# Performance work log

Hardware: AMD Instinct MI355X
Metric: run time of the kernel (lower is better)

The kernel has to match this reference:

```python
import jax, jax.numpy as jnp
import numpy as np

K = 3          # kernel_size
DEG_P = 6      # numerator coeffs (order 5)
DEG_Q = 4      # denominator coeffs (powers 1..4)


def setup_inputs() -> dict:
    key = jax.random.key(0)
    k1, k2, k3 = jax.random.split(key, 3)
    B, Cin, Cout, H, W = 4, 16, 16, 64, 64
    x = jax.random.normal(k1, (B, Cin, H, W), dtype=jnp.float32)
    # per (out_channel f, in_channel c, kernel position p) rational coefficients
    A = jax.random.normal(k2, (Cout, Cin, K * K, DEG_P), dtype=jnp.float32) * 0.1
    Bc = jax.random.normal(k3, (Cout, Cin, K * K, DEG_Q), dtype=jnp.float32) * 0.1
    return {"x": x, "A": A, "Bc": Bc}


def reference(x, A, Bc):
    # x: [B, C, H, W]; A: [F, C, K*K, 6]; Bc: [F, C, K*K, 4]
    B, C, H, W = x.shape
    pad = (K - 1) // 2
    xp = jnp.pad(x, ((0, 0), (0, 0), (pad, pad), (pad, pad)))
    # sliding windows, one slice per kernel offset -> [K*K, B, C, H, W]
    wins = jnp.stack([xp[:, :, i:i + H, j:j + W]
                      for i in range(K) for j in range(K)])
    # powers x^0..x^5 -> [K*K, B, C, H, W, 6]
    pw = wins[..., None] ** jnp.arange(DEG_P, dtype=x.dtype)
    P = jnp.einsum('pbchwi,fcpi->fpbchw', pw, A)
    Q = 1.0 + jnp.abs(jnp.einsum('pbchwi,fcpi->fpbchw', pw[..., 1:1 + DEG_Q], Bc))
    # sum over kernel positions (p) and input channels (c) -> [F, B, H, W]
    out = jnp.sum(P / Q, axis=(1, 3))
    return jnp.transpose(out, (1, 0, 2, 3))  # [B, F, H, W]
```

## Files before the change

kernel.cpp:

```cpp
#include <hip/hip_runtime.h>


#define BB   4
#define CIN  16
#define COUT 16
#define HH   64
#define WW   64

__global__ __launch_bounds__(256) void KAConv_kernel(
    const float* __restrict__ x,
    const float* __restrict__ A,
    const float* __restrict__ Bc,
    float* __restrict__ out)
{
    const int blk   = blockIdx.x;
    const int htile = blk & 15;
    const int f     = (blk >> 4) & 15;
    const int b     = blk >> 8;

    const int t = threadIdx.x;
    const int w = t & 63;
    const int h = (htile << 2) + (t >> 6);

    const float* __restrict__ xb = x  + b * (CIN * HH * WW);
    const float* __restrict__ Af = A  + f * (CIN * 9 * 6);
    const float* __restrict__ Bf = Bc + f * (CIN * 9 * 4);

    float acc = 0.0f;

    for (int c = 0; c < CIN; ++c) {
        const float* __restrict__ xc = xb + c * (HH * WW);

        float v[9];
        #pragma unroll
        for (int i = 0; i < 3; ++i) {
            const int hh = h + i - 1;
            #pragma unroll
            for (int j = 0; j < 3; ++j) {
                const int ww2 = w + j - 1;
                const bool ok = (hh >= 0) & (hh < HH) & (ww2 >= 0) & (ww2 < WW);
                v[i * 3 + j] = ok ? xc[hh * WW + ww2] : 0.0f;
            }
        }

        const float* __restrict__ Ac = Af + c * (9 * 6);
        const float* __restrict__ Bq = Bf + c * (9 * 4);

        #pragma unroll
        for (int p = 0; p < 9; ++p) {
            const float vv = v[p];
            const float* __restrict__ a  = Ac + p * 6;
            const float* __restrict__ bq = Bq + p * 4;

            float P = a[5];
            P = fmaf(P, vv, a[4]);
            P = fmaf(P, vv, a[3]);
            P = fmaf(P, vv, a[2]);
            P = fmaf(P, vv, a[1]);
            P = fmaf(P, vv, a[0]);

            float Qs = bq[3];
            Qs = fmaf(Qs, vv, bq[2]);
            Qs = fmaf(Qs, vv, bq[1]);
            Qs = fmaf(Qs, vv, bq[0]);
            Qs *= vv;

            const float Q = 1.0f + fabsf(Qs);
            acc = fmaf(P, __builtin_amdgcn_rcpf(Q), acc);
        }
    }

    out[((b * COUT + f) * HH + h) * WW + w] = acc;
}

extern "C" void kernel_launch(void* const* d_in, const int* in_sizes, int n_in,
                              void* d_out, int out_size, void* d_ws, size_t ws_size,
                              hipStream_t stream) {
    const float* x  = (const float*)d_in[0];
    const float* A  = (const float*)d_in[1];
    const float* Bc = (const float*)d_in[2];
    float* out = (float*)d_out;

    const int grid = BB * COUT * (HH / 4);
    KAConv_kernel<<<grid, 256, 0, stream>>>(x, A, Bc, out);
}
```

Measured before the change: 23.77 us.

## Compute two output rows per thread and reorder block index mapping

Each thread now computes two vertically adjacent output rows, loading a 4x3 window instead of two 3x3 windows and reusing the coefficient loads across both rows. The grid is halved (512 blocks), and f becomes the fastest-varying block index so neighbouring blocks share the same x tile. This cuts redundant input and coefficient loads per output and adds ILP, at the cost of fewer blocks (lower occupancy across the 256 CUs) and more registers.

```diff
diff --git a/kernel.cpp b/kernel.cpp
--- a/kernel.cpp
+++ b/kernel.cpp
@@ -14,63 +14,73 @@
     float* __restrict__ out)
 {
     const int blk   = blockIdx.x;
-    const int htile = blk & 15;
-    const int f     = (blk >> 4) & 15;
-    const int b     = blk >> 8;
+    const int f     = blk & 15;
+    const int rtile = (blk >> 4) & 7;
+    const int b     = blk >> 7;
 
-    const int t = threadIdx.x;
-    const int w = t & 63;
-    const int h = (htile << 2) + (t >> 6);
+    const int t    = threadIdx.x;
+    const int w    = t & 63;
+    const int warp = t >> 6;
+    const int r0   = (rtile << 3) + (warp << 1);
+    const int r1   = r0 + 1;
 
     const float* __restrict__ xb = x  + b * (CIN * HH * WW);
     const float* __restrict__ Af = A  + f * (CIN * 9 * 6);
     const float* __restrict__ Bf = Bc + f * (CIN * 9 * 4);
 
-    float acc = 0.0f;
+    float acc0 = 0.0f, acc1 = 0.0f;
 
     for (int c = 0; c < CIN; ++c) {
         const float* __restrict__ xc = xb + c * (HH * WW);
 
-        float v[9];
+        float vv[4][3];
         #pragma unroll
-        for (int i = 0; i < 3; ++i) {
-            const int hh = h + i - 1;
+        for (int ri = 0; ri < 4; ++ri) {
+            const int hh  = r0 - 1 + ri;
+            const bool okh = (hh >= 0) & (hh < HH);
             #pragma unroll
             for (int j = 0; j < 3; ++j) {
-                const int ww2 = w + j - 1;
-                const bool ok = (hh >= 0) & (hh < HH) & (ww2 >= 0) & (ww2 < WW);
-                v[i * 3 + j] = ok ? xc[hh * WW + ww2] : 0.0f;
+                const int wj = w + j - 1;
+                const bool ok = okh & (wj >= 0) & (wj < WW);
+                vv[ri][j] = ok ? xc[hh * WW + wj] : 0.0f;
             }
         }
 
-        const float* __restrict__ Ac = Af + c * (9 * 6);
-        const float* __restrict__ Bq = Bf + c * (9 * 4);
+        const float* __restrict__ Ac = Af + c * 54;
+        const float* __restrict__ Bq = Bf + c * 36;
 
         #pragma unroll
         for (int p = 0; p < 9; ++p) {
-            const float vv = v[p];
+            const int i = p / 3;
+            const int j = p % 3;
+            const float va = vv[i][j];
+            const float vb = vv[i + 1][j];
             const float* __restrict__ a  = Ac + p * 6;
             const float* __restrict__ bq = Bq + p * 4;
 
-            float P = a[5];
-            P = fmaf(P, vv, a[4]);
-            P = fmaf(P, vv, a[3]);
-            P = fmaf(P, vv, a[2]);
-            P = fmaf(P, vv, a[1]);
-            P = fmaf(P, vv, a[0]);
+            float P0 = a[5], P1 = a[5];
+            P0 = fmaf(P0, va, a[4]);  P1 = fmaf(P1, vb, a[4]);
+            P0 = fmaf(P0, va, a[3]);  P1 = fmaf(P1, vb, a[3]);
+            P0 = fmaf(P0, va, a[2]);  P1 = fmaf(P1, vb, a[2]);
+            P0 = fmaf(P0, va, a[1]);  P1 = fmaf(P1, vb, a[1]);
+            P0 = fmaf(P0, va, a[0]);  P1 = fmaf(P1, vb, a[0]);
 
-            float Qs = bq[3];
-            Qs = fmaf(Qs, vv, bq[2]);
-            Qs = fmaf(Qs, vv, bq[1]);
-            Qs = fmaf(Qs, vv, bq[0]);
-            Qs *= vv;
+            float q0 = bq[3], q1 = bq[3];
+            q0 = fmaf(q0, va, bq[2]); q1 = fmaf(q1, vb, bq[2]);
+            q0 = fmaf(q0, va, bq[1]); q1 = fmaf(q1, vb, bq[1]);
+            q0 = fmaf(q0, va, bq[0]); q1 = fmaf(q1, vb, bq[0]);
+            q0 *= va;                 q1 *= vb;
 
-            const float Q = 1.0f + fabsf(Qs);
-            acc = fmaf(P, __builtin_amdgcn_rcpf(Q), acc);
+            const float d0 = 1.0f + fabsf(q0);
+            const float d1 = 1.0f + fabsf(q1);
+            acc0 = fmaf(P0, __builtin_amdgcn_rcpf(d0), acc0);
+            acc1 = fmaf(P1, __builtin_amdgcn_rcpf(d1), acc1);
         }
     }
 
-    out[((b * COUT + f) * HH + h) * WW + w] = acc;
+    float* __restrict__ of = out + ((b * COUT + f) * HH) * WW + w;
+    of[r0 * WW] = acc0;
+    of[r1 * WW] = acc1;
 }
 
 extern "C" void kernel_launch(void* const* d_in, const int* in_sizes, int n_in,
@@ -81,6 +91,6 @@
     const float* Bc = (const float*)d_in[2];
     float* out = (float*)d_out;
 
-    const int grid = BB * COUT * (HH / 4);
+    const int grid = BB * (HH / 8) * COUT;
     KAConv_kernel<<<grid, 256, 0, stream>>>(x, A, Bc, out);
 }
```

Measured after the change: 22.39 us. 1.06x faster.

## Parallelize over input channels per block and reduce across channels in shared memory

Applied to the files above, without the earlier changes.

Restructures the grid so each 1024-thread block handles one output row of one batch, with one wavefront per input channel. Each thread loads its 3x3 window once and loops over all output channels, using wave-uniform coefficient addresses via readfirstlane. Per-channel partial sums go into a 64KB LDS buffer and are reduced after a barrier. This removes the repeated input window loads across output channels. In exchange it adds shared-memory traffic and a block-wide sync, and 64KB of LDS per block limits occupancy.

```diff
diff --git a/kernel.cpp b/kernel.cpp
--- a/kernel.cpp
+++ b/kernel.cpp
@@ -7,70 +7,73 @@
 #define HH   64
 #define WW   64
 
-__global__ __launch_bounds__(256) void KAConv_kernel(
+__global__ __launch_bounds__(1024, 4) void KAConv_kernel(
     const float* __restrict__ x,
     const float* __restrict__ A,
     const float* __restrict__ Bc,
     float* __restrict__ out)
 {
-    const int blk   = blockIdx.x;
-    const int htile = blk & 15;
-    const int f     = (blk >> 4) & 15;
-    const int b     = blk >> 8;
+    const int blk = blockIdx.x;
+    const int row = blk & 63;
+    const int b   = blk >> 6;
 
-    const int t = threadIdx.x;
-    const int w = t & 63;
-    const int h = (htile << 2) + (t >> 6);
+    const int tid = threadIdx.x;
+    const int c   = __builtin_amdgcn_readfirstlane(tid >> 6);
+    const int w   = tid & 63;
 
-    const float* __restrict__ xb = x  + b * (CIN * HH * WW);
-    const float* __restrict__ Af = A  + f * (CIN * 9 * 6);
-    const float* __restrict__ Bf = Bc + f * (CIN * 9 * 4);
+    __shared__ float sRed[CIN][COUT][WW];
 
-    float acc = 0.0f;
-
-    for (int c = 0; c < CIN; ++c) {
-        const float* __restrict__ xc = xb + c * (HH * WW);
-
-        float v[9];
+    const float* __restrict__ xc = x + (b * CIN + c) * (HH * WW);
+    float win[3][3];
+    #pragma unroll
+    for (int i = 0; i < 3; ++i) {
+        const int hh   = row - 1 + i;
+        const bool okh = (hh >= 0) & (hh < HH);
         #pragma unroll
-        for (int i = 0; i < 3; ++i) {
-            const int hh = h + i - 1;
-            #pragma unroll
-            for (int j = 0; j < 3; ++j) {
-                const int ww2 = w + j - 1;
-                const bool ok = (hh >= 0) & (hh < HH) & (ww2 >= 0) & (ww2 < WW);
-                v[i * 3 + j] = ok ? xc[hh * WW + ww2] : 0.0f;
-            }
-        }
-
-        const float* __restrict__ Ac = Af + c * (9 * 6);
-        const float* __restrict__ Bq = Bf + c * (9 * 4);
-
-        #pragma unroll
-        for (int p = 0; p < 9; ++p) {
-            const float vv = v[p];
-            const float* __restrict__ a  = Ac + p * 6;
-            const float* __restrict__ bq = Bq + p * 4;
-
-            float P = a[5];
-            P = fmaf(P, vv, a[4]);
-            P = fmaf(P, vv, a[3]);
-            P = fmaf(P, vv, a[2]);
-            P = fmaf(P, vv, a[1]);
-            P = fmaf(P, vv, a[0]);
-
-            float Qs = bq[3];
-            Qs = fmaf(Qs, vv, bq[2]);
-            Qs = fmaf(Qs, vv, bq[1]);
-            Qs = fmaf(Qs, vv, bq[0]);
-            Qs *= vv;
-
-            const float Q = 1.0f + fabsf(Qs);
-            acc = fmaf(P, __builtin_amdgcn_rcpf(Q), acc);
+        for (int j = 0; j < 3; ++j) {
+            const int wj  = w - 1 + j;
+            const bool ok = okh & (wj >= 0) & (wj < WW);
+            win[i][j] = ok ? xc[hh * WW + wj] : 0.0f;
         }
     }
 
-    out[((b * COUT + f) * HH + h) * WW + w] = acc;
+    #pragma unroll 1
+    for (int f = 0; f < COUT; ++f) {
+        const float* __restrict__ Ac = A  + (f * CIN + c) * 54;
+        const float* __restrict__ Bq = Bc + (f * CIN + c) * 36;
+
+        float facc = 0.0f;
+        #pragma unroll
+        for (int p = 0; p < 9; ++p) {
+            const float v = win[p / 3][p % 3];
+            const float a0 = Ac[p*6+0], a1 = Ac[p*6+1], a2 = Ac[p*6+2];
+            const float a3 = Ac[p*6+3], a4 = Ac[p*6+4], a5 = Ac[p*6+5];
+            const float b1 = Bq[p*4+0], b2 = Bq[p*4+1];
+            const float b3 = Bq[p*4+2], b4 = Bq[p*4+3];
+
+            float P = a5;
+            P = fmaf(P, v, a4); P = fmaf(P, v, a3); P = fmaf(P, v, a2);
+            P = fmaf(P, v, a1); P = fmaf(P, v, a0);
+
+            float q = b4;
+            q = fmaf(q, v, b3); q = fmaf(q, v, b2); q = fmaf(q, v, b1);
+            q *= v;
+
+            const float d = 1.0f + fabsf(q);
+            facc = fmaf(P, __builtin_amdgcn_rcpf(d), facc);
+        }
+        sRed[c][f][w] = facc;
+    }
+    __syncthreads();
+
+    {
+        const int f  = tid >> 6;
+        const int px = tid & 63;
+        float s = 0.0f;
+        #pragma unroll
+        for (int k = 0; k < CIN; ++k) s += sRed[k][f][px];
+        out[((b * COUT + f) * HH + row) * WW + px] = s;
+    }
 }
 
 extern "C" void kernel_launch(void* const* d_in, const int* in_sizes, int n_in,
@@ -81,6 +84,6 @@
     const float* Bc = (const float*)d_in[2];
     float* out = (float*)d_out;
 
-    const int grid = BB * COUT * (HH / 4);
-    KAConv_kernel<<<grid, 256, 0, stream>>>(x, A, Bc, out);
+    const int grid = BB * HH;
+    KAConv_kernel<<<grid, 1024, 0, stream>>>(x, A, Bc, out);
 }
```

After: 23.41 us. About the same (-1.5%).
